# Optimization experiments

Hardware: AMD Instinct MI355X
Metric: run time of the kernel (lower is better)

## Reference

```python
import jax, jax.numpy as jnp
import numpy as np
import math

G = 96        # grid cells per axis (domain_size)
N = 400000    # particles, one per occupied cell
CELL = 0.05   # cell size == particle radius parameter d


def setup_inputs():
    rng = np.random.default_rng(0)
    cells = rng.permutation(G ** 3)[:N]
    cz_i = cells // (G * G)
    cy_i = (cells // G) % G
    cx_i = cells % G
    key = jax.random.key(0)
    ks = jax.random.split(key, 6)

    def pos(k, idx):
        jitter = jax.random.uniform(k, (N,), minval=-0.3, maxval=0.3)
        return (jnp.asarray(idx, jnp.float32) + jitter) * CELL

    x = pos(ks[0], cx_i)
    y = pos(ks[1], cy_i)
    z = pos(ks[2], cz_i)
    vx = jax.random.normal(ks[3], (N,), jnp.float32) * 0.1
    vy = jax.random.normal(ks[4], (N,), jnp.float32) * 0.1
    vz = jax.random.normal(ks[5], (N,), jnp.float32) * 0.1
    restitution = 0.5
    alpha = -math.log(restitution) / math.pi
    gamma = alpha / math.sqrt(alpha ** 2 + 1.0)
    kn = 600000.0
    m = 4.0 / 3.0 * 3.1415 * CELL ** 3 * 2700.0
    eta = 2.0 * gamma * math.sqrt(kn * m / 2.0)
    return dict(
        compressed_x_grid=x, compressed_y_grid=y, compressed_z_grid=z,
        compressed_vx_grid=vx, compressed_vy_grid=vy, compressed_vz_grid=vz,
        d=CELL, kn=kn, damping_coefficient_Eta=eta,
        friction_coefficient=0.5, dt=0.001,
        input_shape=(1, 1, G, G, G), filter_size=5)


def reference(compressed_x_grid, compressed_y_grid, compressed_z_grid,
              compressed_vx_grid, compressed_vy_grid, compressed_vz_grid,
              d, kn, damping_coefficient_Eta, friction_coefficient, dt,
              input_shape, filter_size):
    Gz, Gy, Gx = input_shape[2], input_shape[3], input_shape[4]
    n = compressed_x_grid.shape[0]
    eps = jnp.float32(1e-4)
    two_d = 2.0 * d

    # cell indices (one particle per cell, as in the torch module)
    cx = jnp.round(compressed_x_grid / d).astype(jnp.int32)
    cy = jnp.round(compressed_y_grid / d).astype(jnp.int32)
    cz = jnp.round(compressed_z_grid / d).astype(jnp.int32)

    def scatter(v):
        return jnp.zeros((Gz, Gy, Gx), v.dtype).at[cz, cy, cx].set(v)

    xg = scatter(compressed_x_grid)
    yg = scatter(compressed_y_grid)
    zg = scatter(compressed_z_grid)
    vxg = scatter(compressed_vx_grid)
    vyg = scatter(compressed_vy_grid)
    vzg = scatter(compressed_vz_grid)

    half = filter_size // 2
    shifts = jnp.array([[kk - half, jj - half, ii - half]
                        for ii in range(filter_size)
                        for jj in range(filter_size)
                        for kk in range(filter_size)], dtype=jnp.int32)

    def body(carry, shift):
        fxc, fyc, fzc, fxd, fyd, fzd = carry

        def gat(g):
            r = jnp.roll(g, shift[0], axis=0)
            r = jnp.roll(r, shift[1], axis=1)
            r = jnp.roll(r, shift[2], axis=2)
            return r[cz, cy, cx]

        # diff = grid - rolled grid, gathered at the particle cells.
        # grid[cell] holds the particle's own value, so gather(self) == value.
        dx = compressed_x_grid - gat(xg)
        dy = compressed_y_grid - gat(yg)
        dz = compressed_z_grid - gat(zg)
        dvx = compressed_vx_grid - gat(vxg)
        dvy = compressed_vy_grid - gat(vyg)
        dvz = compressed_vz_grid - gat(vzg)

        dist = jnp.sqrt(dx * dx + dy * dy + dz * dz)
        den = jnp.maximum(eps, dist)
        vn = (dvx * dx + dvy * dy + dvz * dz) / den  # normal relative velocity
        ov = dist < two_d                            # overlap mask
        fcol = kn * (dist - two_d) / den             # Hookean repulsion / den
        fdmp = damping_coefficient_Eta * vn / den    # normal damping / den

        fxc = fxc + jnp.where(ov, fcol * dx, 0.0)
        fyc = fyc + jnp.where(ov, fcol * dy, 0.0)
        fzc = fzc + jnp.where(ov, fcol * dz, 0.0)
        fxd = fxd + jnp.where(ov, fdmp * dx, 0.0)
        fyd = fyd + jnp.where(ov, fdmp * dy, 0.0)
        fzd = fzd + jnp.where(ov, fdmp * dz, 0.0)
        return (fxc, fyc, fzc, fxd, fyd, fzd), None

    zeros = jnp.zeros((n,), jnp.float32)
    carry, _ = jax.lax.scan(body, (zeros, zeros, zeros, zeros, zeros, zeros), shifts)
    fxc, fyc, fzc, fxd, fyd, fzd = carry

    # wall (boundary) spring forces, domain extent = grid_dim * cell_size
    dsx, dsy, dsz = Gx * d, Gy * d, Gz * d

    def wall(p, ds):
        lo = jnp.where((p != 0.0) & (p < d), kn * (d - p), 0.0)
        hi = jnp.where(p > ds - two_d, kn * (p - ds + two_d), 0.0)
        return lo - hi

    fbx = wall(compressed_x_grid, dsx)
    fby = wall(compressed_y_grid, dsy)
    fbz = wall(compressed_z_grid, dsz)

    return jnp.stack([fxc, fyc, fzc, fxd, fyd, fzd, fbx, fby, fbz])
```

## Files before the change

kernel.cpp:

```cpp
#include <hip/hip_runtime.h>

#define GDIM 96
#define GCELLS (GDIM * GDIM * GDIM)
#define HX 12
#define HY 12
#define HZ 8
#define HCELLS (HX * HY * HZ)
#define TCELLS 256
#define NTX 12
#define NTY 12
#define NTZ 24
#define NBLK (NTX * NTY * NTZ)
#define EMPTY32 0xDEDEDEDEu


__global__ __launch_bounds__(256) void scatter_k(
    const float* __restrict__ x, const float* __restrict__ y, const float* __restrict__ z,
    const float* __restrict__ vx, const float* __restrict__ vy, const float* __restrict__ vz,
    const float* __restrict__ dp, const float* __restrict__ knp,
    uint4* __restrict__ grid, float* __restrict__ out, int n)
{
    int i = blockIdx.x * blockDim.x + threadIdx.x;
    if (i >= n) return;
    float d = dp[0], kn = knp[0];
    float invd = 1.0f / d;
    float fx = x[i], fy = y[i], fz = z[i];
    float pxc = fx * invd, pyc = fy * invd, pzc = fz * invd;
    int cx = __float2int_rn(pxc);
    int cy = __float2int_rn(pyc);
    int cz = __float2int_rn(pzc);

    uint4 r0, r1;
    r0.x = __float_as_uint(pxc);
    r0.y = __float_as_uint(pyc);
    r0.z = __float_as_uint(pzc);
    r0.w = __float_as_uint(vx[i]);
    r1.x = __float_as_uint(vy[i]);
    r1.y = __float_as_uint(vz[i]);
    r1.z = 0u;
    r1.w = (unsigned int)(i + 1);
    size_t cell = (size_t)(cz * GDIM + cy) * GDIM + cx;
    grid[2 * cell + 0] = r0;
    grid[2 * cell + 1] = r1;

    float two_d = 2.0f * d, ds = (float)GDIM * d;
    size_t N = (size_t)n;
    float lox = (fx != 0.0f && fx < d) ? kn * (d - fx) : 0.0f;
    float hix = (fx > ds - two_d) ? kn * (fx - ds + two_d) : 0.0f;
    float loy = (fy != 0.0f && fy < d) ? kn * (d - fy) : 0.0f;
    float hiy = (fy > ds - two_d) ? kn * (fy - ds + two_d) : 0.0f;
    float loz = (fz != 0.0f && fz < d) ? kn * (d - fz) : 0.0f;
    float hiz = (fz > ds - two_d) ? kn * (fz - ds + two_d) : 0.0f;
    out[6 * N + i] = lox - hix;
    out[7 * N + i] = loy - hiy;
    out[8 * N + i] = loz - hiz;
}

#define NROW(IZ, IY, WD, X0) { \
    int rb = ((lz + IZ) * HY + (ly + IY)) * HX + lx; \
    _Pragma("unroll") \
    for (int k = 0; k < WD; ++k) { \
        int idx = rb + (X0 + k); \
        float4 np = P[idx]; \
        float2 nw = Wv[idx]; \
        float dx = xi - np.x, dy = yi - np.y, dz = zi - np.z; \
        float dvx = vxi - np.w, dvy = vyi - nw.x, dvz = vzi - nw.y; \
        float s = fmaf(dx, dx, fmaf(dy, dy, dz * dz)); \
        float t = fmaxf(s, 4e-6f); \
        float rinv = __builtin_amdgcn_rsqf(t); \
        float dist = s * rinv; \
        float dot = fmaf(dvx, dx, fmaf(dvy, dy, dvz * dz)); \
        bool ov = dist < 2.0f; \
        float fc = ov ? (dist - 2.0f) * rinv : 0.0f; \
        float fd = ov ? dot * rinv * rinv : 0.0f; \
        fxc = fmaf(fc, dx, fxc); fyc = fmaf(fc, dy, fyc); fzc = fmaf(fc, dz, fzc); \
        fxd = fmaf(fd, dx, fxd); fyd = fmaf(fd, dy, fyd); fzd = fmaf(fd, dz, fzd); \
    } }

__global__ __launch_bounds__(512, 8) void force_tile_k(
    const uint4* __restrict__ grid,
    const float* __restrict__ dp, const float* __restrict__ knp,
    const float* __restrict__ etap, float* __restrict__ out, int n)
{
    __shared__ union {
        struct { float4 P[HCELLS]; float2 W[HCELLS]; } g;
        float pbuf[6 * TCELLS];
    } U;
    __shared__ unsigned int llist[TCELLS];
    __shared__ int lcount;

    float4* P = U.g.P;
    float2* Wv = U.g.W;

    int tid = threadIdx.x;
    int bid = blockIdx.x;
    int tileid = (bid & 7) * (NBLK / 8) + (bid >> 3);
    int tx = tileid % NTX;
    int ty = (tileid / NTX) % NTY;
    int tz = tileid / (NTX * NTY);
    int bx = tx * 8 - 2, by = ty * 8 - 2, bz = tz * 4 - 2;

    if (tid == 0) lcount = 0;
    __syncthreads();

    int lane = tid & 63;
    for (int h = tid; h < HCELLS; h += 512) {
        int hx = h % HX;
        int hy = (h / HX) % HY;
        int hz = h / (HX * HY);
        int gx = bx + hx; if (gx < 0) gx += GDIM; else if (gx >= GDIM) gx -= GDIM;
        int gy = by + hy; if (gy < 0) gy += GDIM; else if (gy >= GDIM) gy -= GDIM;
        int gz = bz + hz; if (gz < 0) gz += GDIM; else if (gz >= GDIM) gz -= GDIM;
        size_t gcell = (size_t)(gz * GDIM + gy) * GDIM + gx;
        uint4 r0 = grid[2 * gcell];
        uint4 r1 = grid[2 * gcell + 1];
        P[h] = make_float4(__uint_as_float(r0.x), __uint_as_float(r0.y),
                           __uint_as_float(r0.z), __uint_as_float(r0.w));
        Wv[h] = make_float2(__uint_as_float(r1.x), __uint_as_float(r1.y));
        bool inter = hx >= 2 && hx < 10 && hy >= 2 && hy < 10 && hz >= 2 && hz < 6;
        bool occ = inter && (r1.w != EMPTY32);
        unsigned long long m = __ballot(occ);
        int base = 0;
        if (lane == 0 && m) base = atomicAdd(&lcount, __popcll(m));
        base = __shfl(base, 0);
        if (occ) {
            int off = __popcll(m & ((1ull << lane) - 1ull));
            int ic = ((hz - 2) * 8 + (hy - 2)) * 8 + (hx - 2);
            llist[base + off] = (r1.w << 8) | (unsigned int)ic;
        }
    }
    __syncthreads();

    float d = dp[0], kn = knp[0], eta = etap[0];
    int cnt = lcount;
    size_t N = (size_t)n;
    int base = tid & 255;
    bool isg0 = tid < 256;
    bool active = base < cnt;

    int lc = 0, pid = -1;
    if (active) {
        unsigned int e = llist[base];
        lc = (int)(e & 255u);
        pid = (int)(e >> 8) - 1;
    }
    int lx = lc & 7, ly = (lc >> 3) & 7, lz = lc >> 6;
    int hc = ((lz + 2) * HY + (ly + 2)) * HX + (lx + 2);
    float4 own = P[hc];
    float2 ownw = Wv[hc];
    float xi = own.x, yi = own.y, zi = own.z;
    float vxi = own.w, vyi = ownw.x, vzi = ownw.y;

    float fxc = 0, fyc = 0, fzc = 0, fxd = 0, fyd = 0, fzd = 0;
    if (active) {
        if (isg0) {
            NROW(0,0,1,2) NROW(0,1,3,1) NROW(0,2,5,0) NROW(0,3,3,1) NROW(0,4,1,2)
            NROW(1,0,3,1) NROW(1,1,5,0) NROW(1,2,5,0) NROW(1,3,5,0) NROW(1,4,3,1)
            NROW(2,0,5,0) NROW(2,1,5,0)

            float ss = xi * xi + yi * yi + zi * zi;
            if (ss < 4.0f) {
                int cntE = 0;
#pragma unroll 1
                for (int iz = 0; iz < 5; ++iz)
#pragma unroll 1
                    for (int iy = 0; iy < 5; ++iy)
#pragma unroll 1
                        for (int ix = 0; ix < 5; ++ix) {
                            int hc2 = ((lz + iz) * HY + (ly + iy)) * HX + (lx + ix);
                            if (__float_as_uint(P[hc2].x) == EMPTY32) ++cntE;
                        }
                if (cntE) {
                    float t = fmaxf(ss, 4e-6f);
                    float rinv = __builtin_amdgcn_rsqf(t);
                    float dist = ss * rinv;
                    if (dist < 2.0f) {
                        float fcE = (dist - 2.0f) * rinv;
                        float dotE = vxi * xi + vyi * yi + vzi * zi;
                        float fdE = dotE * rinv * rinv;
                        float c = (float)cntE;
                        fxc = fmaf(c * fcE, xi, fxc); fyc = fmaf(c * fcE, yi, fyc); fzc = fmaf(c * fcE, zi, fzc);
                        fxd = fmaf(c * fdE, xi, fxd); fyd = fmaf(c * fdE, yi, fyd); fzd = fmaf(c * fdE, zi, fzd);
                    }
                }
            }
        } else {
            NROW(2,2,5,0) NROW(2,3,5,0) NROW(2,4,5,0)
            NROW(3,0,3,1) NROW(3,1,5,0) NROW(3,2,5,0) NROW(3,3,5,0) NROW(3,4,3,1)
            NROW(4,0,1,2) NROW(4,1,3,1) NROW(4,2,5,0) NROW(4,3,3,1) NROW(4,4,1,2)
        }
    }

    __syncthreads();
    if (!isg0 && active) {
        U.pbuf[0 * TCELLS + base] = fxc;
        U.pbuf[1 * TCELLS + base] = fyc;
        U.pbuf[2 * TCELLS + base] = fzc;
        U.pbuf[3 * TCELLS + base] = fxd;
        U.pbuf[4 * TCELLS + base] = fyd;
        U.pbuf[5 * TCELLS + base] = fzd;
    }
    __syncthreads();
    if (isg0 && active) {
        float kd = kn * d;
        out[0 * N + pid] = (fxc + U.pbuf[0 * TCELLS + base]) * kd;
        out[1 * N + pid] = (fyc + U.pbuf[1 * TCELLS + base]) * kd;
        out[2 * N + pid] = (fzc + U.pbuf[2 * TCELLS + base]) * kd;
        out[3 * N + pid] = (fxd + U.pbuf[3 * TCELLS + base]) * eta;
        out[4 * N + pid] = (fyd + U.pbuf[4 * TCELLS + base]) * eta;
        out[5 * N + pid] = (fzd + U.pbuf[5 * TCELLS + base]) * eta;
    }
}

extern "C" void kernel_launch(void* const* d_in, const int* in_sizes, int n_in,
                              void* d_out, int out_size, void* d_ws, size_t ws_size,
                              hipStream_t stream)
{
    const float* x  = (const float*)d_in[0];
    const float* y  = (const float*)d_in[1];
    const float* z  = (const float*)d_in[2];
    const float* vx = (const float*)d_in[3];
    const float* vy = (const float*)d_in[4];
    const float* vz = (const float*)d_in[5];
    const float* dp   = (const float*)d_in[6];
    const float* knp  = (const float*)d_in[7];
    const float* etap = (const float*)d_in[8];
    int n = in_sizes[0];

    uint4* grid = (uint4*)d_ws;

    hipMemsetAsync(d_ws, 0xDE, (size_t)GCELLS * 32, stream);

    int blocks = (n + 255) / 256;
    scatter_k<<<blocks, 256, 0, stream>>>(x, y, z, vx, vy, vz, dp, knp, grid, (float*)d_out, n);
    force_tile_k<<<NBLK, 512, 0, stream>>>(grid, dp, knp, etap, (float*)d_out, n);
}
```

Measured before the change: 99.14 us.

## Enlarge force tiles to 8x8x8 cubes with padded halo and looped passes

Each block now covers an 8x8x8 interior tile with a 12x12x12 halo instead of an 8x8x4 tile with a 12x12x8 halo. That lowers the halo-to-interior load ratio and halves the block count. Up to 512 particles are processed in a loop of 256-particle passes, still split between two half-blocks by stencil half. The halo row stride is padded to 13 to reduce LDS bank conflicts, and neighbour loads per row are batched before computing. The larger LDS footprint lowers occupancy (launch bounds 8 to 6), and the extra pass loop adds barriers.

```diff
diff --git a/kernel.cpp b/kernel.cpp
--- a/kernel.cpp
+++ b/kernel.cpp
@@ -2,15 +2,14 @@
 
 #define GDIM 96
 #define GCELLS (GDIM * GDIM * GDIM)
-#define HX 12
+#define HX 13
 #define HY 12
-#define HZ 8
+#define HZ 12
 #define HCELLS (HX * HY * HZ)
-#define TCELLS 256
-#define NTX 12
-#define NTY 12
-#define NTZ 24
-#define NBLK (NTX * NTY * NTZ)
+#define LHC (12 * 12 * 12)
+#define TCELLS 512
+#define NT 12
+#define NBLK (NT * NT * NT)
 #define EMPTY32 0xDEDEDEDEu
 
 
@@ -56,68 +55,69 @@
     out[8 * N + i] = loz - hiz;
 }
 
-#define NROW(IZ, IY, WD, X0) { \
-    int rb = ((lz + IZ) * HY + (ly + IY)) * HX + lx; \
-    _Pragma("unroll") \
-    for (int k = 0; k < WD; ++k) { \
-        int idx = rb + (X0 + k); \
-        float4 np = P[idx]; \
-        float2 nw = Wv[idx]; \
-        float dx = xi - np.x, dy = yi - np.y, dz = zi - np.z; \
-        float dvx = vxi - np.w, dvy = vyi - nw.x, dvz = vzi - nw.y; \
-        float s = fmaf(dx, dx, fmaf(dy, dy, dz * dz)); \
-        float t = fmaxf(s, 4e-6f); \
-        float rinv = __builtin_amdgcn_rsqf(t); \
-        float dist = s * rinv; \
-        float dot = fmaf(dvx, dx, fmaf(dvy, dy, dvz * dz)); \
-        bool ov = dist < 2.0f; \
-        float fc = ov ? (dist - 2.0f) * rinv : 0.0f; \
-        float fd = ov ? dot * rinv * rinv : 0.0f; \
-        fxc = fmaf(fc, dx, fxc); fyc = fmaf(fc, dy, fyc); fzc = fmaf(fc, dz, fzc); \
-        fxd = fmaf(fd, dx, fxd); fyd = fmaf(fd, dy, fyd); fzd = fmaf(fd, dz, fzd); \
-    } }
-
-__global__ __launch_bounds__(512, 8) void force_tile_k(
+#define BODY(np, nw) { \
+    float dx = xi - np.x, dy = yi - np.y, dz = zi - np.z; \
+    float dvx = vxi - np.w, dvy = vyi - nw.x, dvz = vzi - nw.y; \
+    float s = fmaf(dx, dx, fmaf(dy, dy, dz * dz)); \
+    float t = fmaxf(s, 4e-6f); \
+    float rinv = __builtin_amdgcn_rsqf(t); \
+    float dist = s * rinv; \
+    float dot = fmaf(dvx, dx, fmaf(dvy, dy, dvz * dz)); \
+    bool ov = dist < 2.0f; \
+    float fc = ov ? (dist - 2.0f) * rinv : 0.0f; \
+    float fd = ov ? dot * rinv * rinv : 0.0f; \
+    fxc = fmaf(fc, dx, fxc); fyc = fmaf(fc, dy, fyc); fzc = fmaf(fc, dz, fzc); \
+    fxd = fmaf(fd, dx, fxd); fyd = fmaf(fd, dy, fyd); fzd = fmaf(fd, dz, fzd); }
+
+#define NROW5(IZ, IY) { int rb = ((lz + IZ) * HY + (ly + IY)) * HX + lx; \
+    float4 q0 = P[rb], q1 = P[rb+1], q2 = P[rb+2], q3 = P[rb+3], q4 = P[rb+4]; \
+    float2 w0 = Wv[rb], w1 = Wv[rb+1], w2 = Wv[rb+2], w3 = Wv[rb+3], w4 = Wv[rb+4]; \
+    BODY(q0, w0) BODY(q1, w1) BODY(q2, w2) BODY(q3, w3) BODY(q4, w4) }
+#define NROW3(IZ, IY) { int rb = ((lz + IZ) * HY + (ly + IY)) * HX + lx; \
+    float4 q1 = P[rb+1], q2 = P[rb+2], q3 = P[rb+3]; \
+    float2 w1 = Wv[rb+1], w2 = Wv[rb+2], w3 = Wv[rb+3]; \
+    BODY(q1, w1) BODY(q2, w2) BODY(q3, w3) }
+#define NROW1(IZ, IY) { int rb = ((lz + IZ) * HY + (ly + IY)) * HX + lx; \
+    float4 q2 = P[rb+2]; float2 w2 = Wv[rb+2]; BODY(q2, w2) }
+
+__global__ __launch_bounds__(512, 6) void force_tile_k(
     const uint4* __restrict__ grid,
     const float* __restrict__ dp, const float* __restrict__ knp,
     const float* __restrict__ etap, float* __restrict__ out, int n)
 {
-    __shared__ union {
-        struct { float4 P[HCELLS]; float2 W[HCELLS]; } g;
-        float pbuf[6 * TCELLS];
-    } U;
+    __shared__ float4 P[HCELLS];
+    __shared__ float2 Wv[HCELLS];
+    __shared__ float pbuf[6 * 256];
     __shared__ unsigned int llist[TCELLS];
     __shared__ int lcount;
-
-    float4* P = U.g.P;
-    float2* Wv = U.g.W;
 
     int tid = threadIdx.x;
     int bid = blockIdx.x;
     int tileid = (bid & 7) * (NBLK / 8) + (bid >> 3);
-    int tx = tileid % NTX;
-    int ty = (tileid / NTX) % NTY;
-    int tz = tileid / (NTX * NTY);
-    int bx = tx * 8 - 2, by = ty * 8 - 2, bz = tz * 4 - 2;
+    int tx = tileid % NT;
+    int ty = (tileid / NT) % NT;
+    int tz = tileid / (NT * NT);
+    int bx = tx * 8 - 2, by = ty * 8 - 2, bz = tz * 8 - 2;
 
     if (tid == 0) lcount = 0;
     __syncthreads();
 
     int lane = tid & 63;
-    for (int h = tid; h < HCELLS; h += 512) {
-        int hx = h % HX;
-        int hy = (h / HX) % HY;
-        int hz = h / (HX * HY);
+    for (int h = tid; h < LHC; h += 512) {
+        int hx = h % 12;
+        int hy = (h / 12) % 12;
+        int hz = h / 144;
         int gx = bx + hx; if (gx < 0) gx += GDIM; else if (gx >= GDIM) gx -= GDIM;
         int gy = by + hy; if (gy < 0) gy += GDIM; else if (gy >= GDIM) gy -= GDIM;
         int gz = bz + hz; if (gz < 0) gz += GDIM; else if (gz >= GDIM) gz -= GDIM;
         size_t gcell = (size_t)(gz * GDIM + gy) * GDIM + gx;
         uint4 r0 = grid[2 * gcell];
         uint4 r1 = grid[2 * gcell + 1];
-        P[h] = make_float4(__uint_as_float(r0.x), __uint_as_float(r0.y),
-                           __uint_as_float(r0.z), __uint_as_float(r0.w));
-        Wv[h] = make_float2(__uint_as_float(r1.x), __uint_as_float(r1.y));
-        bool inter = hx >= 2 && hx < 10 && hy >= 2 && hy < 10 && hz >= 2 && hz < 6;
+        int hi = (hz * HY + hy) * HX + hx;
+        P[hi] = make_float4(__uint_as_float(r0.x), __uint_as_float(r0.y),
+                            __uint_as_float(r0.z), __uint_as_float(r0.w));
+        Wv[hi] = make_float2(__uint_as_float(r1.x), __uint_as_float(r1.y));
+        bool inter = hx >= 2 && hx < 10 && hy >= 2 && hy < 10 && hz >= 2 && hz < 10;
         bool occ = inter && (r1.w != EMPTY32);
         unsigned long long m = __ballot(occ);
         int base = 0;
@@ -125,8 +125,8 @@
         base = __shfl(base, 0);
         if (occ) {
             int off = __popcll(m & ((1ull << lane) - 1ull));
-            int ic = ((hz - 2) * 8 + (hy - 2)) * 8 + (hx - 2);
-            llist[base + off] = (r1.w << 8) | (unsigned int)ic;
+            int ic = (((hz - 2) * 8 + (hy - 2)) * 8) + (hx - 2);
+            llist[base + off] = (r1.w << 9) | (unsigned int)ic;
         }
     }
     __syncthreads();
@@ -136,79 +136,80 @@
     size_t N = (size_t)n;
     int base = tid & 255;
     bool isg0 = tid < 256;
-    bool active = base < cnt;
-
-    int lc = 0, pid = -1;
-    if (active) {
-        unsigned int e = llist[base];
-        lc = (int)(e & 255u);
-        pid = (int)(e >> 8) - 1;
-    }
-    int lx = lc & 7, ly = (lc >> 3) & 7, lz = lc >> 6;
-    int hc = ((lz + 2) * HY + (ly + 2)) * HX + (lx + 2);
-    float4 own = P[hc];
-    float2 ownw = Wv[hc];
-    float xi = own.x, yi = own.y, zi = own.z;
-    float vxi = own.w, vyi = ownw.x, vzi = ownw.y;
-
-    float fxc = 0, fyc = 0, fzc = 0, fxd = 0, fyd = 0, fzd = 0;
-    if (active) {
-        if (isg0) {
-            NROW(0,0,1,2) NROW(0,1,3,1) NROW(0,2,5,0) NROW(0,3,3,1) NROW(0,4,1,2)
-            NROW(1,0,3,1) NROW(1,1,5,0) NROW(1,2,5,0) NROW(1,3,5,0) NROW(1,4,3,1)
-            NROW(2,0,5,0) NROW(2,1,5,0)
-
-            float ss = xi * xi + yi * yi + zi * zi;
-            if (ss < 4.0f) {
-                int cntE = 0;
+    int nit = (cnt + 255) >> 8;
+
+    for (int it = 0; it < nit; ++it) {
+        int ip = it * 256 + base;
+        bool act = ip < cnt;
+        unsigned int e = llist[act ? ip : 0];
+        int lc = (int)(e & 511u);
+        int pid = (int)(e >> 9) - 1;
+        int lx = lc & 7, ly = (lc >> 3) & 7, lz = lc >> 6;
+        int hc = ((lz + 2) * HY + (ly + 2)) * HX + (lx + 2);
+        float4 own = P[hc];
+        float2 ownw = Wv[hc];
+        float xi = own.x, yi = own.y, zi = own.z;
+        float vxi = own.w, vyi = ownw.x, vzi = ownw.y;
+
+        float fxc = 0, fyc = 0, fzc = 0, fxd = 0, fyd = 0, fzd = 0;
+        if (act) {
+            if (isg0) {
+                NROW1(0,0) NROW3(0,1) NROW5(0,2) NROW3(0,3) NROW1(0,4)
+                NROW3(1,0) NROW5(1,1) NROW5(1,2) NROW5(1,3) NROW3(1,4)
+                NROW5(2,0) NROW5(2,1)
+
+                float ss = xi * xi + yi * yi + zi * zi;
+                if (ss < 4.0f) {
+                    int cntE = 0;
 #pragma unroll 1
-                for (int iz = 0; iz < 5; ++iz)
+                    for (int iz = 0; iz < 5; ++iz)
 #pragma unroll 1
-                    for (int iy = 0; iy < 5; ++iy)
+                        for (int iy = 0; iy < 5; ++iy)
 #pragma unroll 1
-                        for (int ix = 0; ix < 5; ++ix) {
-                            int hc2 = ((lz + iz) * HY + (ly + iy)) * HX + (lx + ix);
-                            if (__float_as_uint(P[hc2].x) == EMPTY32) ++cntE;
+                            for (int ix = 0; ix < 5; ++ix) {
+                                int hc2 = ((lz + iz) * HY + (ly + iy)) * HX + (lx + ix);
+                                if (__float_as_uint(P[hc2].x) == EMPTY32) ++cntE;
+                            }
+                    if (cntE) {
+                        float t = fmaxf(ss, 4e-6f);
+                        float rinv = __builtin_amdgcn_rsqf(t);
+                        float dist = ss * rinv;
+                        if (dist < 2.0f) {
+                            float fcE = (dist - 2.0f) * rinv;
+                            float dotE = vxi * xi + vyi * yi + vzi * zi;
+                            float fdE = dotE * rinv * rinv;
+                            float c = (float)cntE;
+                            fxc = fmaf(c * fcE, xi, fxc); fyc = fmaf(c * fcE, yi, fyc); fzc = fmaf(c * fcE, zi, fzc);
+                            fxd = fmaf(c * fdE, xi, fxd); fyd = fmaf(c * fdE, yi, fyd); fzd = fmaf(c * fdE, zi, fzd);
                         }
-                if (cntE) {
-                    float t = fmaxf(ss, 4e-6f);
-                    float rinv = __builtin_amdgcn_rsqf(t);
-                    float dist = ss * rinv;
-                    if (dist < 2.0f) {
-                        float fcE = (dist - 2.0f) * rinv;
-                        float dotE = vxi * xi + vyi * yi + vzi * zi;
-                        float fdE = dotE * rinv * rinv;
-                        float c = (float)cntE;
-                        fxc = fmaf(c * fcE, xi, fxc); fyc = fmaf(c * fcE, yi, fyc); fzc = fmaf(c * fcE, zi, fzc);
-                        fxd = fmaf(c * fdE, xi, fxd); fyd = fmaf(c * fdE, yi, fyd); fzd = fmaf(c * fdE, zi, fzd);
                     }
                 }
+            } else {
+                NROW5(2,2) NROW5(2,3) NROW5(2,4)
+                NROW3(3,0) NROW5(3,1) NROW5(3,2) NROW5(3,3) NROW3(3,4)
+                NROW1(4,0) NROW3(4,1) NROW5(4,2) NROW3(4,3) NROW1(4,4)
             }
-        } else {
-            NROW(2,2,5,0) NROW(2,3,5,0) NROW(2,4,5,0)
-            NROW(3,0,3,1) NROW(3,1,5,0) NROW(3,2,5,0) NROW(3,3,5,0) NROW(3,4,3,1)
-            NROW(4,0,1,2) NROW(4,1,3,1) NROW(4,2,5,0) NROW(4,3,3,1) NROW(4,4,1,2)
-        }
-    }
-
-    __syncthreads();
-    if (!isg0 && active) {
-        U.pbuf[0 * TCELLS + base] = fxc;
-        U.pbuf[1 * TCELLS + base] = fyc;
-        U.pbuf[2 * TCELLS + base] = fzc;
-        U.pbuf[3 * TCELLS + base] = fxd;
-        U.pbuf[4 * TCELLS + base] = fyd;
-        U.pbuf[5 * TCELLS + base] = fzd;
-    }
-    __syncthreads();
-    if (isg0 && active) {
-        float kd = kn * d;
-        out[0 * N + pid] = (fxc + U.pbuf[0 * TCELLS + base]) * kd;
-        out[1 * N + pid] = (fyc + U.pbuf[1 * TCELLS + base]) * kd;
-        out[2 * N + pid] = (fzc + U.pbuf[2 * TCELLS + base]) * kd;
-        out[3 * N + pid] = (fxd + U.pbuf[3 * TCELLS + base]) * eta;
-        out[4 * N + pid] = (fyd + U.pbuf[4 * TCELLS + base]) * eta;
-        out[5 * N + pid] = (fzd + U.pbuf[5 * TCELLS + base]) * eta;
+        }
+
+        __syncthreads();
+        if (!isg0 && act) {
+            pbuf[0 * 256 + base] = fxc;
+            pbuf[1 * 256 + base] = fyc;
+            pbuf[2 * 256 + base] = fzc;
+            pbuf[3 * 256 + base] = fxd;
+            pbuf[4 * 256 + base] = fyd;
+            pbuf[5 * 256 + base] = fzd;
+        }
+        __syncthreads();
+        if (isg0 && act) {
+            float kd = kn * d;
+            out[0 * N + pid] = (fxc + pbuf[0 * 256 + base]) * kd;
+            out[1 * N + pid] = (fyc + pbuf[1 * 256 + base]) * kd;
+            out[2 * N + pid] = (fzc + pbuf[2 * 256 + base]) * kd;
+            out[3 * N + pid] = (fxd + pbuf[3 * 256 + base]) * eta;
+            out[4 * N + pid] = (fyd + pbuf[4 * 256 + base]) * eta;
+            out[5 * N + pid] = (fzd + pbuf[5 * 256 + base]) * eta;
+        }
     }
 }
 
```

Result: faster. 85.79 us (-13.5%).
